# Performance work log

Hardware: AMD Instinct MI355X
Metric: run time of the kernel (lower is better)

The kernel has to match this reference:

```python
import jax, jax.numpy as jnp
import numpy as np

NEG = -9e15
N_NODES, IN_DIM, H1, H2, HEADS, DEC, N_EDGES, B_PAIRS = 4096, 512, 256, 128, 4, 512, 131072, 4096


def setup_inputs() -> dict:
    key = jax.random.key(0)
    ks = jax.random.split(key, 24)
    d = {}
    d["x_o"] = jax.random.normal(ks[0], (N_NODES, IN_DIM), jnp.float32)
    d["x_a"] = jax.random.normal(ks[1], (N_NODES, IN_DIM), jnp.float32)
    d["edge_index"] = jax.random.randint(ks[2], (2, N_EDGES), 0, N_NODES)
    d["idx"] = jax.random.randint(ks[3], (2, B_PAIRS), 0, N_NODES)
    # GAT layer 1 (in=IN_DIM, out=H1), per-head stacked params
    d["W1"] = jax.random.normal(ks[4], (HEADS, IN_DIM, H1)) * (IN_DIM ** -0.5)
    d["a1"] = jax.random.normal(ks[5], (HEADS, 2 * H1)) * 0.1
    d["lin1"] = jax.random.normal(ks[6], (HEADS * H1, H1)) * ((HEADS * H1) ** -0.5)
    d["res1"] = jax.random.normal(ks[7], (IN_DIM, H1)) * (IN_DIM ** -0.5)
    # GAT layer 2 (in=H1, out=H2)
    d["W2"] = jax.random.normal(ks[8], (HEADS, H1, H2)) * (H1 ** -0.5)
    d["a2"] = jax.random.normal(ks[9], (HEADS, 2 * H2)) * 0.1
    d["lin2"] = jax.random.normal(ks[10], (HEADS * H2, H2)) * ((HEADS * H2) ** -0.5)
    d["res2"] = jax.random.normal(ks[11], (H1, H2)) * (H1 ** -0.5)
    # heads
    d["mlp1_w"] = jax.random.normal(ks[12], (H2, H2)) * (H2 ** -0.5)
    d["mlp1_b"] = jnp.zeros((H2,))
    d["disc_w"] = jax.random.normal(ks[13], (H2, H2)) * (H2 ** -0.5)
    d["disc_b"] = jnp.zeros(())
    d["dec1_w"] = jax.random.normal(ks[14], (2 * H2, DEC)) * ((2 * H2) ** -0.5)
    d["dec1_b"] = jnp.zeros((DEC,))
    d["dec2_w"] = jax.random.normal(ks[15], (DEC, 1)) * (DEC ** -0.5)
    d["dec2_b"] = jnp.zeros((1,))
    d["adv_w"] = jax.random.normal(ks[16], (H2, H2)) * (H2 ** -0.5)
    d["adv_b"] = jnp.zeros((H2,))
    return d


def _gat_residual_layer(h, mask, W, a, lin, res):
    # W: [H, Fin, Fo], a: [H, 2*Fo]. e_ij = leakyrelu(Wh_i . a[:Fo] + Wh_j . a[Fo:])
    # (algebraically identical to the NxN all-pairs concat @ a in the torch code).
    def head(Wk, ak):
        Wh = h @ Wk                      # [N, Fo]
        Fo = Wk.shape[1]
        src = Wh @ ak[:Fo]               # [N]
        dst = Wh @ ak[Fo:]               # [N]
        e = jax.nn.leaky_relu(src[:, None] + dst[None, :], 0.2)  # [N, N]
        att = jax.nn.softmax(jnp.where(mask, e, NEG), axis=1)
        return jax.nn.elu(att @ Wh)      # [N, Fo]

    heads = jax.vmap(head)(W, a)         # [H, N, Fo]
    Hn, N, Fo = heads.shape
    concat = jnp.transpose(heads, (1, 0, 2)).reshape(N, Hn * Fo)
    mh = jax.nn.elu(concat @ lin)
    return jax.nn.relu(mh + h @ res)     # relu(relu(x)) == relu(x); dropout off in eval


def reference(x_o, x_a, W1, a1, lin1, res1, W2, a2, lin2, res2,
              mlp1_w, mlp1_b, disc_w, disc_b, dec1_w, dec1_b,
              dec2_w, dec2_b, adv_w, adv_b, edge_index, idx):
    N = x_o.shape[0]
    mask = jnp.zeros((N, N), jnp.bool_).at[edge_index[0], edge_index[1]].set(True)

    def encode(x):
        h = _gat_residual_layer(x, mask, W1, a1, lin1, res1)
        h = _gat_residual_layer(h, mask, W2, a2, lin2, res2)
        return h

    x2_o = encode(x_o)                   # [N, H2]
    x2_o_a = encode(x_a)

    h_os = jax.nn.sigmoid(x2_o.mean(0)) @ mlp1_w + mlp1_b      # [H2]
    h_os_a = jax.nn.sigmoid(x2_o_a.mean(0)) @ mlp1_w + mlp1_b

    def disc(c, h_pl, h_mi):  # Bilinear(h, c) with out=1
        sc1 = (h_pl @ disc_w) @ c + disc_b
        sc2 = (h_mi @ disc_w) @ c + disc_b
        return jnp.stack([sc1, sc2], axis=1)                    # [N, 2]

    ret_os = disc(h_os, x2_o, x2_o_a)
    ret_os_a = disc(h_os_a, x2_o_a, x2_o)

    # extract_entities, default branch (task_type not in {LDA, MDA, LMI})
    entity1 = x2_o[idx[0]]
    entity2 = x2_o[idx[1]]
    z = jnp.concatenate([entity1, entity2], axis=1)             # [B, 2*H2]
    hdec = jax.nn.relu(z @ dec1_w + dec1_b)
    log1 = hdec @ dec2_w + dec2_b                               # [B, 1]
    log = jax.nn.sigmoid(log1)

    sc_1 = (x2_o @ adv_w + adv_b).sum(1)[None, :]               # [1, N]
    sc_2 = (x2_o_a @ adv_w + adv_b).sum(1)[None, :]
    logits = jnp.concatenate([sc_1, sc_2], axis=1)              # [1, 2N]

    return (log, ret_os, ret_os_a, x2_o, logits, log1)
```

## Files before the change

kernel.cpp:

```cpp
#include <hip/hip_runtime.h>
#include <stdint.h>

#define N_NODES 4096
#define N_EDGES 131072

typedef __attribute__((ext_vector_type(8))) short short8;
typedef __attribute__((ext_vector_type(4))) float floatx4;

__device__ __forceinline__ float bf2f(unsigned short u) {
  union { unsigned u; float f; } v; v.u = ((unsigned)u) << 16; return v.f;
}
__device__ __forceinline__ unsigned short f2bf(float f) {
  union { float f; unsigned u; } v; v.f = f;
  unsigned r = 0x7FFFu + ((v.u >> 16) & 1u);
  return (unsigned short)((v.u + r) >> 16);
}
__device__ __forceinline__ float wredsum(float x) {
#pragma unroll
  for (int d = 32; d >= 1; d >>= 1) x += __shfl_xor(x, d);
  return x;
}
__device__ __forceinline__ float wredmax(float x) {
#pragma unroll
  for (int d = 32; d >= 1; d >>= 1) x = fmaxf(x, __shfl_xor(x, d));
  return x;
}
__device__ __forceinline__ void gload16(const void* g, void* l) {
  __builtin_amdgcn_global_load_lds(
      (const __attribute__((address_space(1))) unsigned*)g,
      (__attribute__((address_space(3))) unsigned*)l, 16, 0, 0);
}

__global__ __launch_bounds__(256) void gemm128(
    const unsigned short* __restrict__ A, const unsigned short* __restrict__ Bt,
    int M, int N, int K, unsigned short* __restrict__ Cb,
    const float* __restrict__ avec, float* __restrict__ sdv, int FO) {
  __shared__ __align__(16) unsigned short As[128 * 32];
  __shared__ __align__(16) unsigned short Bs[128 * 32];
  const int t = threadIdx.x, lane = t & 63, w = t >> 6;
  const int wr = w >> 1, wc = w & 1;
  const int n0 = blockIdx.x * 128, m0 = blockIdx.y * 128;
  floatx4 acc[4][4] = {};
  const int arow = t >> 2;
  const int schunk = (t & 3) ^ ((arow >> 1) & 3);

  for (int kt = 0; kt < K; kt += 32) {
    __syncthreads();
    gload16(A + (size_t)(m0 + arow) * K + kt + schunk * 8, &As[t * 8]);
    gload16(A + (size_t)(m0 + 64 + arow) * K + kt + schunk * 8, &As[(256 + t) * 8]);
    gload16(Bt + (size_t)(n0 + arow) * K + kt + schunk * 8, &Bs[t * 8]);
    gload16(Bt + (size_t)(n0 + 64 + arow) * K + kt + schunk * 8, &Bs[(256 + t) * 8]);
    __syncthreads();
    short8 af[4], bfr[4];
    const int koff = lane >> 4;
#pragma unroll
    for (int m = 0; m < 4; ++m) {
      const int r = wr * 64 + (lane & 15) + m * 16;
      af[m] = *(const short8*)&As[r * 32 + ((koff ^ ((r >> 1) & 3)) << 3)];
    }
#pragma unroll
    for (int n = 0; n < 4; ++n) {
      const int r = wc * 64 + (lane & 15) + n * 16;
      bfr[n] = *(const short8*)&Bs[r * 32 + ((koff ^ ((r >> 1) & 3)) << 3)];
    }
#pragma unroll
    for (int m = 0; m < 4; ++m)
#pragma unroll
      for (int n = 0; n < 4; ++n)
        acc[m][n] = __builtin_amdgcn_mfma_f32_16x16x32_bf16(af[m], bfr[n], acc[m][n], 0, 0, 0);
  }

  const int rb = m0 + wr * 64 + (lane >> 4) * 4;
  const int cb = n0 + wc * 64 + (lane & 15);
#pragma unroll
  for (int m = 0; m < 4; ++m)
#pragma unroll
    for (int n = 0; n < 4; ++n) {
      const int col = cb + n * 16;
#pragma unroll
      for (int r = 0; r < 4; ++r) {
        const int row = rb + m * 16 + r;
        Cb[(size_t)row * N + col] = f2bf(acc[m][n][r]);
      }
    }

  if (avec) {
    const int h = n0 / FO;
    const int cw0 = cb - h * FO;
    float as_[4], ad_[4];
#pragma unroll
    for (int n = 0; n < 4; ++n) {
      as_[n] = avec[h * 2 * FO + cw0 + n * 16];
      ad_[n] = avec[h * 2 * FO + FO + cw0 + n * 16];
    }
#pragma unroll
    for (int m = 0; m < 4; ++m)
#pragma unroll
      for (int r = 0; r < 4; ++r) {
        float sp = 0.f, dp = 0.f;
#pragma unroll
        for (int n = 0; n < 4; ++n) {
          sp += acc[m][n][r] * as_[n];
          dp += acc[m][n][r] * ad_[n];
        }
#pragma unroll
        for (int d = 1; d < 16; d <<= 1) {
          sp += __shfl_xor(sp, d);
          dp += __shfl_xor(dp, d);
        }
        if ((lane & 15) == 0) {
          const int row = rb + m * 16 + r;
          atomicAdd(&sdv[row * 8 + h], sp);
          atomicAdd(&sdv[row * 8 + 4 + h], dp);
        }
      }
  }
}

__device__ __forceinline__ void stage64(const unsigned short* __restrict__ G,
                                        unsigned short* lds, int row0, int K,
                                        int kt, int t) {
  const int l0 = t, l1 = t + 256;
  const int r0 = l0 >> 3, c0 = l0 & 7;
  const int r1 = l1 >> 3, c1 = l1 & 7;
  gload16(G + (size_t)(row0 + r0) * K + kt + ((c0 ^ (r0 & 7)) << 3), &lds[l0 * 8]);
  gload16(G + (size_t)(row0 + r1) * K + kt + ((c1 ^ (r1 & 7)) << 3), &lds[l1 * 8]);
}
__device__ __forceinline__ short8 frag64(const unsigned short* lds, int r, int c) {
  return *(const short8*)&lds[r * 64 + ((c ^ (r & 7)) << 3)];
}

template <int EP>
__global__ __launch_bounds__(256) void gemm64(
    const unsigned short* __restrict__ A, const unsigned short* __restrict__ Bt,
    int M, int N, int K, unsigned short* __restrict__ Cb,
    const float* __restrict__ bias) {
  __shared__ __align__(16) unsigned short As[64 * 64];
  __shared__ __align__(16) unsigned short Bs[64 * 64];
  const int t = threadIdx.x, lane = t & 63, w = t >> 6;
  const int wr = w >> 1, wc = w & 1;
  const int n0 = blockIdx.x * 64, m0 = blockIdx.y * 64;
  floatx4 acc[2][2] = {};

  for (int kt = 0; kt < K; kt += 64) {
    __syncthreads();
    stage64(A, As, m0, K, kt, t);
    stage64(Bt, Bs, n0, K, kt, t);
    __syncthreads();
    short8 af[2][2], bfv[2][2];
#pragma unroll
    for (int m = 0; m < 2; ++m) {
      const int ra = wr * 32 + (lane & 15) + m * 16;
#pragma unroll
      for (int kk = 0; kk < 2; ++kk)
        af[m][kk] = frag64(As, ra, (lane >> 4) + kk * 4);
    }
#pragma unroll
    for (int n = 0; n < 2; ++n) {
      const int rb = wc * 32 + (lane & 15) + n * 16;
#pragma unroll
      for (int kk = 0; kk < 2; ++kk)
        bfv[n][kk] = frag64(Bs, rb, (lane >> 4) + kk * 4);
    }
#pragma unroll
    for (int kk = 0; kk < 2; ++kk)
#pragma unroll
      for (int m = 0; m < 2; ++m)
#pragma unroll
        for (int n = 0; n < 2; ++n)
          acc[m][n] = __builtin_amdgcn_mfma_f32_16x16x32_bf16(af[m][kk], bfv[n][kk], acc[m][n], 0, 0, 0);
  }

  const int rb = m0 + wr * 32 + (lane >> 4) * 4;
  const int cb = n0 + wc * 32 + (lane & 15);
#pragma unroll
  for (int m = 0; m < 2; ++m)
#pragma unroll
    for (int n = 0; n < 2; ++n) {
      const int col = cb + n * 16;
#pragma unroll
      for (int r = 0; r < 4; ++r) {
        const int row = rb + m * 16 + r;
        float v = acc[m][n][r];
        if (EP == 4) { v += bias[col]; v = v > 0.f ? v : 0.f; }
        Cb[(size_t)row * N + col] = f2bf(v);
      }
    }
}

template <int EP>
__global__ __launch_bounds__(256) void gemm64dual(
    const unsigned short* __restrict__ A1, const unsigned short* __restrict__ B1t, int K1,
    const unsigned short* __restrict__ A2, const unsigned short* __restrict__ B2t, int K2,
    int N, unsigned short* __restrict__ Cb,
    float* __restrict__ Cfo, float* __restrict__ Cfa) {
  __shared__ __align__(16) unsigned short As[64 * 64];
  __shared__ __align__(16) unsigned short Bs[64 * 64];
  const int t = threadIdx.x, lane = t & 63, w = t >> 6;
  const int wr = w >> 1, wc = w & 1;
  const int n0 = blockIdx.x * 64, m0 = blockIdx.y * 64;
  floatx4 acc[2][2] = {};

#pragma unroll 1
  for (int pass = 0; pass < 2; ++pass) {
    const unsigned short* A = pass ? A2 : A1;
    const unsigned short* Bt = pass ? B2t : B1t;
    const int K = pass ? K2 : K1;
    for (int kt = 0; kt < K; kt += 64) {
      __syncthreads();
      stage64(A, As, m0, K, kt, t);
      stage64(Bt, Bs, n0, K, kt, t);
      __syncthreads();
      short8 af[2][2], bfv[2][2];
#pragma unroll
      for (int m = 0; m < 2; ++m) {
        const int ra = wr * 32 + (lane & 15) + m * 16;
#pragma unroll
        for (int kk = 0; kk < 2; ++kk)
          af[m][kk] = frag64(As, ra, (lane >> 4) + kk * 4);
      }
#pragma unroll
      for (int n = 0; n < 2; ++n) {
        const int rb = wc * 32 + (lane & 15) + n * 16;
#pragma unroll
        for (int kk = 0; kk < 2; ++kk)
          bfv[n][kk] = frag64(Bs, rb, (lane >> 4) + kk * 4);
      }
#pragma unroll
      for (int kk = 0; kk < 2; ++kk)
#pragma unroll
        for (int m = 0; m < 2; ++m)
#pragma unroll
          for (int n = 0; n < 2; ++n)
            acc[m][n] = __builtin_amdgcn_mfma_f32_16x16x32_bf16(af[m][kk], bfv[n][kk], acc[m][n], 0, 0, 0);
    }
    if (pass == 0) {
#pragma unroll
      for (int m = 0; m < 2; ++m)
#pragma unroll
        for (int n = 0; n < 2; ++n)
#pragma unroll
          for (int r = 0; r < 4; ++r) {
            float v = acc[m][n][r];
            acc[m][n][r] = v > 0.f ? v : expm1f(v);
          }
    }
  }

  const int rb = m0 + wr * 32 + (lane >> 4) * 4;
  const int cb = n0 + wc * 32 + (lane & 15);
#pragma unroll
  for (int m = 0; m < 2; ++m)
#pragma unroll
    for (int n = 0; n < 2; ++n) {
      const int col = cb + n * 16;
#pragma unroll
      for (int r = 0; r < 4; ++r) {
        const int row = rb + m * 16 + r;
        float v = acc[m][n][r];
        v = v > 0.f ? v : 0.f;
        if (EP == 0) {
          Cb[(size_t)row * N + col] = f2bf(v);
        } else {
          float* bb = (row < 4096) ? Cfo : Cfa;
          bb[(size_t)(row & 4095) * N + col] = v;
        }
      }
    }
}

__global__ __launch_bounds__(256) void scatter_kernel(
    const int* __restrict__ ei, unsigned long long* __restrict__ mb,
    float* __restrict__ sd1, float* __restrict__ sd2) {
  int b = blockIdx.x;
  if (b < 512) {
    int e = b * 256 + threadIdx.x;
    int r = ei[e], c = ei[N_EDGES + e];
    atomicOr(&mb[(size_t)r * 64 + (c >> 6)], 1ull << (c & 63));
  } else {
    int z = (b - 512) * 256 + threadIdx.x;
    if (z < 65536) sd1[z] = 0.f;
    else sd2[z - 65536] = 0.f;
  }
}

__global__ __launch_bounds__(256) void csr_count(
    const unsigned long long* __restrict__ mb, int* __restrict__ rcnt) {
  int r = blockIdx.x * 256 + threadIdx.x;
  int c = 0;
#pragma unroll 8
  for (int w = 0; w < 64; ++w) c += __popcll(mb[(size_t)r * 64 + w]);
  rcnt[r] = c;
}

__global__ __launch_bounds__(64) void csr_scan(
    const int* __restrict__ rcnt, int* __restrict__ rbase) {
  int l = threadIdx.x;
  int s = 0;
  for (int k = 0; k < 64; ++k) s += rcnt[l * 64 + k];
  int pre = s;
#pragma unroll
  for (int d = 1; d < 64; d <<= 1) {
    int v = __shfl_up(pre, d);
    if (l >= d) pre += v;
  }
  pre -= s;
  int run = pre;
  for (int k = 0; k < 64; ++k) {
    rbase[l * 64 + k] = run;
    run += rcnt[l * 64 + k];
  }
}

__global__ __launch_bounds__(64) void csr_fill(
    const unsigned long long* __restrict__ mb, const int* __restrict__ rbase,
    unsigned short* __restrict__ nbrg) {
  int r = blockIdx.x, t = threadIdx.x;
  unsigned long long wb = mb[(size_t)r * 64 + t];
  int pc = __popcll(wb);
  int inc = pc;
#pragma unroll
  for (int d = 1; d < 64; d <<= 1) {
    int v = __shfl_up(inc, d);
    if (t >= d) inc += v;
  }
  int off = rbase[r] + inc - pc;
  while (wb) {
    int b = __builtin_ctzll(wb);
    nbrg[off++] = (unsigned short)(t * 64 + b);
    wb &= wb - 1;
  }
}

__global__ __launch_bounds__(256) void pack2_kernel(
    const float* W1, const float* lin1, const float* res1, const float* W2,
    const float* lin2, const float* res2, const float* dec1,
    const float* xo, const float* xa,
    unsigned short* dW1, unsigned short* dlin1, unsigned short* dres1,
    unsigned short* dW2, unsigned short* dlin2, unsigned short* dres2,
    unsigned short* ddec1, unsigned short* x16) {
  const int b = blockIdx.x, t = threadIdx.x;
  if (b >= 1248) {
    int ib = b - 1248;
    const float* src = (ib < 512) ? xo : xa;
    unsigned short* dst = x16 + ((ib < 512) ? 0 : (size_t)4096 * 512);
    size_t base = (size_t)(ib & 511) * 4096;
#pragma unroll
    for (int q = 0; q < 4; ++q) {
      size_t o = base + q * 1024 + t * 4;
      float4 v = *(const float4*)&src[o];
      ushort4 u = {f2bf(v.x), f2bf(v.y), f2bf(v.z), f2bf(v.w)};
      *(ushort4*)&dst[o] = u;
    }
    return;
  }
  const float* src; unsigned short* dst; int K, F, nFt, tb;
  if (b < 512)       { int h = b >> 7;        src = W1 + h * 131072; dst = dW1 + h * 131072; K = 512;  F = 256; nFt = 8;  tb = b & 127; }
  else if (b < 768)  {                        src = lin1;            dst = dlin1;            K = 1024; F = 256; nFt = 8;  tb = b - 512; }
  else if (b < 896)  {                        src = res1;            dst = dres1;            K = 512;  F = 256; nFt = 8;  tb = b - 768; }
  else if (b < 1024) { int h = (b - 896) >> 5; src = W2 + h * 32768; dst = dW2 + h * 32768;  K = 256;  F = 128; nFt = 4;  tb = (b - 896) & 31; }
  else if (b < 1088) {                        src = lin2;            dst = dlin2;            K = 512;  F = 128; nFt = 4;  tb = b - 1024; }
  else if (b < 1120) {                        src = res2;            dst = dres2;            K = 256;  F = 128; nFt = 4;  tb = b - 1088; }
  else               {                        src = dec1;            dst = ddec1;            K = 256;  F = 512; nFt = 16; tb = b - 1120; }
  const int k0 = (tb / nFt) * 32, f0 = (tb % nFt) * 32;
  __shared__ float tile[32][33];
  {
    int r = t >> 3, c4 = (t & 7) * 4;
    float4 v = *(const float4*)&src[(size_t)(k0 + r) * F + f0 + c4];
    tile[r][c4] = v.x; tile[r][c4 + 1] = v.y; tile[r][c4 + 2] = v.z; tile[r][c4 + 3] = v.w;
  }
  __syncthreads();
  {
    int f = t >> 3, k4 = (t & 7) * 4;
    ushort4 u;
    u.x = f2bf(tile[k4 + 0][f]); u.y = f2bf(tile[k4 + 1][f]);
    u.z = f2bf(tile[k4 + 2][f]); u.w = f2bf(tile[k4 + 3][f]);
    *(ushort4*)&dst[(size_t)(f0 + f) * K + k0 + k4] = u;
  }
}

template <int FO>
__global__ __launch_bounds__(256) void attn2_kernel(
    const int* __restrict__ rcnt, const int* __restrict__ rbase,
    const unsigned short* __restrict__ nbrg, const float* __restrict__ sd,
    const unsigned short* __restrict__ Wh, unsigned short* __restrict__ outp) {
  constexpr int E = FO / 64;
  constexpr int W = 4 * FO;
  constexpr int CAP = 512;
  __shared__ __align__(16) unsigned short nb[4][CAP + 8];
  __shared__ __align__(16) float wg[4][CAP + 8];
  const int bid = blockIdx.x;
  const int combo = bid & 7, chunk = bid >> 3;
  const int h = combo & 3, e = combo >> 2;
  const int t = threadIdx.x, lane = t & 63, wv = t >> 6;
  const int r = chunk * 4 + wv;
  const int i = e * 4096 + r;
  const int jb = e * 4096;
  const int cnt = rcnt[r], boff = rbase[r];
  const float src_i = sd[(size_t)i * 8 + h];
  float acc[E] = {};
  float inv = 1.f;

  if (cnt > 0) {
    float m = -1e30f;
    for (int nn = lane; nn < cnt; nn += 64) {
      int j = nbrg[boff + nn];
      if (nn < CAP) nb[wv][nn] = (unsigned short)j;
      float x = src_i + sd[(size_t)(jb + j) * 8 + 4 + h];
      m = fmaxf(m, x > 0.f ? x : 0.2f * x);
    }
    m = wredmax(m);
    float ssum = 0.f;
    for (int nn = lane; nn < cnt; nn += 64) {
      int j = nbrg[boff + nn];
      float x = src_i + sd[(size_t)(jb + j) * 8 + 4 + h];
      float ee = x > 0.f ? x : 0.2f * x;
      float g = __expf(ee - m);
      if (nn < CAP) wg[wv][nn] = g;
      ssum += g;
    }
    ssum = wredsum(ssum);
    inv = 1.f / ssum;
    const int limc = cnt < CAP ? cnt : CAP;
    if (lane < 8) { nb[wv][limc + lane] = 0; wg[wv][limc + lane] = 0.f; }
    const int ngroups = (limc + 7) >> 3;
    for (int g = 0; g < ngroups; ++g) {
      const int nn = g * 8;
      ushort4 ja = *(const ushort4*)&nb[wv][nn];
      ushort4 jb4 = *(const ushort4*)&nb[wv][nn + 4];
      float4 wa = *(const float4*)&wg[wv][nn];
      float4 wb4 = *(const float4*)&wg[wv][nn + 4];
      const int js[8] = {ja.x, ja.y, ja.z, ja.w, jb4.x, jb4.y, jb4.z, jb4.w};
      const float ws[8] = {wa.x, wa.y, wa.z, wa.w, wb4.x, wb4.y, wb4.z, wb4.w};
      if constexpr (E == 4) {
        uint2 rv[8];
#pragma unroll
        for (int q = 0; q < 8; ++q)
          rv[q] = *(const uint2*)(Wh + (size_t)(jb + js[q]) * W + h * FO + lane * 4);
#pragma unroll
        for (int q = 0; q < 8; ++q) {
          acc[0] += ws[q] * bf2f((unsigned short)(rv[q].x & 0xffff));
          acc[1] += ws[q] * bf2f((unsigned short)(rv[q].x >> 16));
          acc[2] += ws[q] * bf2f((unsigned short)(rv[q].y & 0xffff));
          acc[3] += ws[q] * bf2f((unsigned short)(rv[q].y >> 16));
        }
      } else {
        unsigned rv[8];
#pragma unroll
        for (int q = 0; q < 8; ++q)
          rv[q] = *(const unsigned*)(Wh + (size_t)(jb + js[q]) * W + h * FO + lane * 2);
#pragma unroll
        for (int q = 0; q < 8; ++q) {
          acc[0] += ws[q] * bf2f((unsigned short)(rv[q] & 0xffff));
          acc[1] += ws[q] * bf2f((unsigned short)(rv[q] >> 16));
        }
      }
    }
    for (int nn = CAP; nn < cnt; ++nn) {
      int j = nbrg[boff + nn];
      float x = src_i + sd[(size_t)(jb + j) * 8 + 4 + h];
      float ee = x > 0.f ? x : 0.2f * x;
      float g = __expf(ee - m);
      const unsigned short* p = Wh + (size_t)(jb + j) * W + h * FO + lane * E;
#pragma unroll
      for (int q = 0; q < E; ++q) acc[q] += g * bf2f(p[q]);
    }
  } else {
    const float wgu = 1.f / 4096.f;
    for (int j = 0; j < N_NODES; ++j) {
      const unsigned short* p = Wh + (size_t)(jb + j) * W + h * FO + lane * E;
#pragma unroll
      for (int q = 0; q < E; ++q) acc[q] += wgu * bf2f(p[q]);
    }
  }
  unsigned short* op = outp + (size_t)i * W + h * FO + lane * E;
#pragma unroll
  for (int q = 0; q < E; ++q) {
    float v = acc[q] * inv;
    op[q] = f2bf(v > 0.f ? v : expm1f(v));
  }
}

__global__ __launch_bounds__(128) void colsum_kernel(
    const float* __restrict__ x2o, const float* __restrict__ x2a,
    float* __restrict__ small) {
  int b = blockIdx.x, f = threadIdx.x;
  const float* x = (b < 64) ? x2o : x2a;
  float* s = (b < 64) ? small : (small + 128);
  int r0 = (b & 63) * 64;
  float acc = 0.f;
  for (int r = 0; r < 64; ++r) acc += x[(size_t)(r0 + r) * 128 + f];
  atomicAdd(&s[f], acc);
}

__global__ __launch_bounds__(128) void finalize_kernel(
    float* __restrict__ small, const float* __restrict__ mlp1_w,
    const float* __restrict__ mlp1_b, const float* __restrict__ disc_w,
    const float* __restrict__ adv_w, const float* __restrict__ adv_b) {
  __shared__ float so[128], sa[128], ho[128], ha[128];
  int f = threadIdx.x;
  so[f] = 1.f / (1.f + __expf(-small[f] * (1.f / 4096.f)));
  sa[f] = 1.f / (1.f + __expf(-small[128 + f] * (1.f / 4096.f)));
  __syncthreads();
  float aco = mlp1_b[f], aca = mlp1_b[f];
  for (int c = 0; c < 128; ++c) {
    aco += so[c] * mlp1_w[c * 128 + f];
    aca += sa[c] * mlp1_w[c * 128 + f];
  }
  ho[f] = aco;
  ha[f] = aca;
  __syncthreads();
  float vo = 0.f, va = 0.f, ar = 0.f;
  for (int c = 0; c < 128; ++c) {
    vo += disc_w[f * 128 + c] * ho[c];
    va += disc_w[f * 128 + c] * ha[c];
    ar += adv_w[f * 128 + c];
  }
  small[256 + f] = vo;
  small[384 + f] = va;
  small[512 + f] = ar;
  if (f == 0) {
    float b = 0.f;
    for (int c = 0; c < 128; ++c) b += adv_b[c];
    small[640] = b;
  }
}

__global__ __launch_bounds__(256) void pernode_kernel(
    const float* __restrict__ x2o, const float* __restrict__ x2a,
    const float* __restrict__ small, const float* __restrict__ disc_b,
    float* __restrict__ out) {
  const float* v_os = small + 256;
  const float* v_a = small + 384;
  const float* adv_rs = small + 512;
  int lane = threadIdx.x & 63, wv = threadIdx.x >> 6;
  int i = blockIdx.x * 4 + wv;
  float2 xo = *(const float2*)&x2o[(size_t)i * 128 + lane * 2];
  float2 xa = *(const float2*)&x2a[(size_t)i * 128 + lane * 2];
  float2 vo = *(const float2*)&v_os[lane * 2];
  float2 va = *(const float2*)&v_a[lane * 2];
  float2 ar = *(const float2*)&adv_rs[lane * 2];
  float poo = wredsum(xo.x * vo.x + xo.y * vo.y);
  float pao = wredsum(xa.x * vo.x + xa.y * vo.y);
  float paa = wredsum(xa.x * va.x + xa.y * va.y);
  float poa = wredsum(xo.x * va.x + xo.y * va.y);
  float pov = wredsum(xo.x * ar.x + xo.y * ar.y);
  float pav = wredsum(xa.x * ar.x + xa.y * ar.y);
  if (lane == 0) {
    float db = disc_b[0], bv = small[640];
    out[4096 + 2 * i] = poo + db;
    out[4096 + 2 * i + 1] = pao + db;
    out[12288 + 2 * i] = paa + db;
    out[12288 + 2 * i + 1] = poa + db;
    out[544768 + i] = pov + bv;
    out[548864 + i] = pav + bv;
  }
}

__global__ __launch_bounds__(256) void gather_kernel(
    const float* __restrict__ x2o, const int* __restrict__ idx,
    unsigned short* __restrict__ z) {
  int i = blockIdx.x, c = threadIdx.x;
  int s = (c < 128) ? idx[i] : idx[4096 + i];
  z[(size_t)i * 256 + c] = f2bf(x2o[(size_t)s * 128 + (c & 127)]);
}

__global__ __launch_bounds__(256) void dec2_kernel(
    const unsigned short* __restrict__ hdec, const float* __restrict__ w2,
    const float* __restrict__ b2, float* __restrict__ out) {
  int lane = threadIdx.x & 63, wv = threadIdx.x >> 6;
  int i = blockIdx.x * 4 + wv;
  float s = 0.f;
#pragma unroll
  for (int q = 0; q < 8; ++q) {
    int f = lane + q * 64;
    s += bf2f(hdec[(size_t)i * 512 + f]) * w2[f];
  }
  s = wredsum(s);
  if (lane == 0) {
    float v = s + b2[0];
    out[552960 + i] = v;
    out[i] = 1.f / (1.f + __expf(-v));
  }
}

extern "C" void kernel_launch(void* const* d_in, const int* in_sizes, int n_in,
                              void* d_out, int out_size, void* d_ws, size_t ws_size,
                              hipStream_t stream) {
  const float* x_o = (const float*)d_in[0];
  const float* x_a = (const float*)d_in[1];
  const int* ei = (const int*)d_in[2];
  const int* idx = (const int*)d_in[3];
  const float* W1 = (const float*)d_in[4];
  const float* a1 = (const float*)d_in[5];
  const float* lin1 = (const float*)d_in[6];
  const float* res1 = (const float*)d_in[7];
  const float* W2 = (const float*)d_in[8];
  const float* a2 = (const float*)d_in[9];
  const float* lin2 = (const float*)d_in[10];
  const float* res2 = (const float*)d_in[11];
  const float* mlp1_w = (const float*)d_in[12];
  const float* mlp1_b = (const float*)d_in[13];
  const float* disc_w = (const float*)d_in[14];
  const float* disc_b = (const float*)d_in[15];
  const float* dec1_w = (const float*)d_in[16];
  const float* dec1_b = (const float*)d_in[17];
  const float* dec2_w = (const float*)d_in[18];
  const float* dec2_b = (const float*)d_in[19];
  const float* adv_w = (const float*)d_in[20];
  const float* adv_b = (const float*)d_in[21];
  float* out = (float*)d_out;

  char* w = (char*)d_ws;
  size_t off = 0;
  auto alloc = [&](size_t b) {
    char* p = w + off;
    off += (b + 255) & ~(size_t)255;
    return p;
  };
  unsigned long long* mb = (unsigned long long*)alloc((size_t)4096 * 64 * 8);
  unsigned short* x16 = (unsigned short*)alloc((size_t)8192 * 512 * 2);
  unsigned short* Wh1 = (unsigned short*)alloc((size_t)8192 * 1024 * 2);
  unsigned short* ho1 = (unsigned short*)alloc((size_t)8192 * 1024 * 2);
  unsigned short* h1 = (unsigned short*)alloc((size_t)8192 * 256 * 2);
  unsigned short* Wh2 = (unsigned short*)alloc((size_t)8192 * 512 * 2);
  unsigned short* ho2 = (unsigned short*)alloc((size_t)8192 * 512 * 2);
  float* x2a = (float*)alloc((size_t)4096 * 128 * 4);
  float* sd1 = (float*)alloc((size_t)8192 * 8 * 4);
  float* sd2 = (float*)alloc((size_t)8192 * 8 * 4);
  float* small = (float*)alloc(1024 * 4);
  int* rcnt = (int*)alloc(4096 * 4);
  int* rbase = (int*)alloc(4096 * 4);
  unsigned short* nbrg = (unsigned short*)alloc((size_t)(N_EDGES + 64) * 2);
  unsigned short* tW1 = (unsigned short*)alloc((size_t)524288 * 2);
  unsigned short* tlin1 = (unsigned short*)alloc((size_t)262144 * 2);
  unsigned short* tres1 = (unsigned short*)alloc((size_t)131072 * 2);
  unsigned short* tW2 = (unsigned short*)alloc((size_t)131072 * 2);
  unsigned short* tlin2 = (unsigned short*)alloc((size_t)65536 * 2);
  unsigned short* tres2 = (unsigned short*)alloc((size_t)32768 * 2);
  unsigned short* tdec1 = (unsigned short*)alloc((size_t)131072 * 2);
  unsigned short* z16 = (unsigned short*)alloc((size_t)4096 * 256 * 2);
  unsigned short* hdec = (unsigned short*)alloc((size_t)4096 * 512 * 2);

  hipMemsetAsync(mb, 0, (size_t)4096 * 64 * 8, stream);
  hipMemsetAsync(small, 0, 1024, stream);
  scatter_kernel<<<1024, 256, 0, stream>>>(ei, mb, sd1, sd2);
  pack2_kernel<<<2272, 256, 0, stream>>>(W1, lin1, res1, W2, lin2, res2, dec1_w,
                                         x_o, x_a, tW1, tlin1, tres1, tW2,
                                         tlin2, tres2, tdec1, x16);
  csr_count<<<16, 256, 0, stream>>>(mb, rcnt);
  csr_scan<<<1, 64, 0, stream>>>(rcnt, rbase);
  csr_fill<<<4096, 64, 0, stream>>>(mb, rbase, nbrg);

  float* x2o_out = out + 20480;

  gemm128<<<dim3(8, 64), 256, 0, stream>>>(x16, tW1, 8192, 1024, 512, Wh1, a1, sd1, 256);
  attn2_kernel<256><<<8192, 256, 0, stream>>>(rcnt, rbase, nbrg, sd1, Wh1, ho1);
  gemm64dual<0><<<dim3(4, 128), 256, 0, stream>>>(ho1, tlin1, 1024, x16, tres1, 512, 256, h1, nullptr, nullptr);
  gemm128<<<dim3(4, 64), 256, 0, stream>>>(h1, tW2, 8192, 512, 256, Wh2, a2, sd2, 128);
  attn2_kernel<128><<<8192, 256, 0, stream>>>(rcnt, rbase, nbrg, sd2, Wh2, ho2);
  gemm64dual<1><<<dim3(2, 128), 256, 0, stream>>>(ho2, tlin2, 512, h1, tres2, 256, 128, nullptr, x2o_out, x2a);

  colsum_kernel<<<128, 128, 0, stream>>>(x2o_out, x2a, small);
  finalize_kernel<<<1, 128, 0, stream>>>(small, mlp1_w, mlp1_b, disc_w, adv_w, adv_b);
  pernode_kernel<<<1024, 256, 0, stream>>>(x2o_out, x2a, small, disc_b, out);
  gather_kernel<<<4096, 256, 0, stream>>>(x2o_out, idx, z16);
  gemm64<4><<<dim3(8, 64), 256, 0, stream>>>(z16, tdec1, 4096, 512, 256, hdec, dec1_b);
  dec2_kernel<<<1024, 256, 0, stream>>>(hdec, dec2_w, dec2_b, out);
}
```

Baseline: 229.6 us.

## Add single-pass softmax fast path and scalarize neighbor indices in attention

The attention kernel gains a fast path for rows with at most 64 neighbors that computes max, exp and sum in one pass instead of two loops over the neighbor list. Neighbor indices read from shared memory are made wave-uniform with readfirstlane so row addresses can sit in scalar registers, and bf16 unpacking uses shifts and masks directly. csr_fill now packs four rows per 256-thread block, and expm1f is replaced by __expf(v)-1, which loses a little accuracy near zero. The tail loop for rows longer than CAP moves into the slow branch before the grouped accumulation.

```diff
diff --git a/kernel.cpp b/kernel.cpp
--- a/kernel.cpp
+++ b/kernel.cpp
@@ -242,7 +242,7 @@
 #pragma unroll
           for (int r = 0; r < 4; ++r) {
             float v = acc[m][n][r];
-            acc[m][n][r] = v > 0.f ? v : expm1f(v);
+            acc[m][n][r] = v > 0.f ? v : __expf(v) - 1.f;
           }
     }
   }
@@ -312,10 +312,11 @@
   }
 }
 
-__global__ __launch_bounds__(64) void csr_fill(
+__global__ __launch_bounds__(256) void csr_fill(
     const unsigned long long* __restrict__ mb, const int* __restrict__ rbase,
     unsigned short* __restrict__ nbrg) {
-  int r = blockIdx.x, t = threadIdx.x;
+  int r = blockIdx.x * 4 + (threadIdx.x >> 6);
+  int t = threadIdx.x & 63;
   unsigned long long wb = mb[(size_t)r * 64 + t];
   int pc = __popcll(wb);
   int inc = pc;
@@ -402,27 +403,51 @@
   float inv = 1.f;
 
   if (cnt > 0) {
-    float m = -1e30f;
-    for (int nn = lane; nn < cnt; nn += 64) {
-      int j = nbrg[boff + nn];
-      if (nn < CAP) nb[wv][nn] = (unsigned short)j;
-      float x = src_i + sd[(size_t)(jb + j) * 8 + 4 + h];
-      m = fmaxf(m, x > 0.f ? x : 0.2f * x);
-    }
-    m = wredmax(m);
-    float ssum = 0.f;
-    for (int nn = lane; nn < cnt; nn += 64) {
-      int j = nbrg[boff + nn];
-      float x = src_i + sd[(size_t)(jb + j) * 8 + 4 + h];
-      float ee = x > 0.f ? x : 0.2f * x;
-      float g = __expf(ee - m);
-      if (nn < CAP) wg[wv][nn] = g;
-      ssum += g;
-    }
-    ssum = wredsum(ssum);
-    inv = 1.f / ssum;
     const int limc = cnt < CAP ? cnt : CAP;
-    if (lane < 8) { nb[wv][limc + lane] = 0; wg[wv][limc + lane] = 0.f; }
+    if (cnt <= 64) {
+      int j = 0;
+      float ee = -1e30f;
+      if (lane < cnt) {
+        j = nbrg[boff + lane];
+        float x = src_i + sd[(size_t)(jb + j) * 8 + 4 + h];
+        ee = x > 0.f ? x : 0.2f * x;
+      }
+      float m = wredmax(ee);
+      float g = (lane < cnt) ? __expf(ee - m) : 0.f;
+      nb[wv][lane] = (unsigned short)j;
+      wg[wv][lane] = g;
+      inv = 1.f / wredsum(g);
+    } else {
+      float m = -1e30f;
+      for (int nn = lane; nn < cnt; nn += 64) {
+        int j = nbrg[boff + nn];
+        if (nn < CAP) nb[wv][nn] = (unsigned short)j;
+        float x = src_i + sd[(size_t)(jb + j) * 8 + 4 + h];
+        m = fmaxf(m, x > 0.f ? x : 0.2f * x);
+      }
+      m = wredmax(m);
+      float ssum = 0.f;
+      for (int nn = lane; nn < cnt; nn += 64) {
+        int j = nbrg[boff + nn];
+        float x = src_i + sd[(size_t)(jb + j) * 8 + 4 + h];
+        float ee = x > 0.f ? x : 0.2f * x;
+        float g = __expf(ee - m);
+        if (nn < CAP) wg[wv][nn] = g;
+        ssum += g;
+      }
+      ssum = wredsum(ssum);
+      inv = 1.f / ssum;
+      if (lane < 8) { nb[wv][limc + lane] = 0; wg[wv][limc + lane] = 0.f; }
+      for (int nn = CAP; nn < cnt; ++nn) {
+        int j = nbrg[boff + nn];
+        float x = src_i + sd[(size_t)(jb + j) * 8 + 4 + h];
+        float ee = x > 0.f ? x : 0.2f * x;
+        float g = __expf(ee - m);
+        const unsigned short* p = Wh + (size_t)(jb + j) * W + h * FO + lane * E;
+#pragma unroll
+        for (int q = 0; q < E; ++q) acc[q] += g * bf2f(p[q]);
+      }
+    }
     const int ngroups = (limc + 7) >> 3;
     for (int g = 0; g < ngroups; ++g) {
       const int nn = g * 8;
@@ -430,7 +455,14 @@
       ushort4 jb4 = *(const ushort4*)&nb[wv][nn + 4];
       float4 wa = *(const float4*)&wg[wv][nn];
       float4 wb4 = *(const float4*)&wg[wv][nn + 4];
-      const int js[8] = {ja.x, ja.y, ja.z, ja.w, jb4.x, jb4.y, jb4.z, jb4.w};
+      const int js[8] = {__builtin_amdgcn_readfirstlane((int)ja.x),
+                         __builtin_amdgcn_readfirstlane((int)ja.y),
+                         __builtin_amdgcn_readfirstlane((int)ja.z),
+                         __builtin_amdgcn_readfirstlane((int)ja.w),
+                         __builtin_amdgcn_readfirstlane((int)jb4.x),
+                         __builtin_amdgcn_readfirstlane((int)jb4.y),
+                         __builtin_amdgcn_readfirstlane((int)jb4.z),
+                         __builtin_amdgcn_readfirstlane((int)jb4.w)};
       const float ws[8] = {wa.x, wa.y, wa.z, wa.w, wb4.x, wb4.y, wb4.z, wb4.w};
       if constexpr (E == 4) {
         uint2 rv[8];
@@ -439,10 +471,13 @@
           rv[q] = *(const uint2*)(Wh + (size_t)(jb + js[q]) * W + h * FO + lane * 4);
 #pragma unroll
         for (int q = 0; q < 8; ++q) {
-          acc[0] += ws[q] * bf2f((unsigned short)(rv[q].x & 0xffff));
-          acc[1] += ws[q] * bf2f((unsigned short)(rv[q].x >> 16));
-          acc[2] += ws[q] * bf2f((unsigned short)(rv[q].y & 0xffff));
-          acc[3] += ws[q] * bf2f((unsigned short)(rv[q].y >> 16));
+          union { unsigned u; float f; } l0, h0, l1, h1;
+          l0.u = rv[q].x << 16; h0.u = rv[q].x & 0xffff0000u;
+          l1.u = rv[q].y << 16; h1.u = rv[q].y & 0xffff0000u;
+          acc[0] += ws[q] * l0.f;
+          acc[1] += ws[q] * h0.f;
+          acc[2] += ws[q] * l1.f;
+          acc[3] += ws[q] * h1.f;
         }
       } else {
         unsigned rv[8];
@@ -451,19 +486,12 @@
           rv[q] = *(const unsigned*)(Wh + (size_t)(jb + js[q]) * W + h * FO + lane * 2);
 #pragma unroll
         for (int q = 0; q < 8; ++q) {
-          acc[0] += ws[q] * bf2f((unsigned short)(rv[q] & 0xffff));
-          acc[1] += ws[q] * bf2f((unsigned short)(rv[q] >> 16));
+          union { unsigned u; float f; } l0, h0;
+          l0.u = rv[q] << 16; h0.u = rv[q] & 0xffff0000u;
+          acc[0] += ws[q] * l0.f;
+          acc[1] += ws[q] * h0.f;
         }
       }
-    }
-    for (int nn = CAP; nn < cnt; ++nn) {
-      int j = nbrg[boff + nn];
-      float x = src_i + sd[(size_t)(jb + j) * 8 + 4 + h];
-      float ee = x > 0.f ? x : 0.2f * x;
-      float g = __expf(ee - m);
-      const unsigned short* p = Wh + (size_t)(jb + j) * W + h * FO + lane * E;
-#pragma unroll
-      for (int q = 0; q < E; ++q) acc[q] += g * bf2f(p[q]);
     }
   } else {
     const float wgu = 1.f / 4096.f;
@@ -477,7 +505,7 @@
 #pragma unroll
   for (int q = 0; q < E; ++q) {
     float v = acc[q] * inv;
-    op[q] = f2bf(v > 0.f ? v : expm1f(v));
+    op[q] = f2bf(v > 0.f ? v : __expf(v) - 1.f);
   }
 }
 
@@ -650,7 +678,7 @@
                                          tlin2, tres2, tdec1, x16);
   csr_count<<<16, 256, 0, stream>>>(mb, rcnt);
   csr_scan<<<1, 64, 0, stream>>>(rcnt, rbase);
-  csr_fill<<<4096, 64, 0, stream>>>(mb, rbase, nbrg);
+  csr_fill<<<1024, 256, 0, stream>>>(mb, rbase, nbrg);
 
   float* x2o_out = out + 20480;
 
```

Measured after the change: 216.7 us. 5.7% less time.
